# Kernel optimization log

Hardware: AMD Instinct MI355X
Metric: run time of the kernel (lower is better)

Reference implementation:

```python
import jax, jax.numpy as jnp
import numpy as np

TOTAL_BITS = 16
FRAC_BITS = 8
SCALE = float(2 ** FRAC_BITS)
MINV = -(2.0 ** (TOTAL_BITS - 1)) / SCALE          # -128.0
MAXV = (2.0 ** (TOTAL_BITS - 1) - 1.0) / SCALE     # 127.99609375
BN_EPS = 1e-5


def fp_quantize(x):
    """Fixed-point fake-quant: clamp to representable range, round to nearest
    multiple of 2^-frac_bits. Rounding uses straight-through estimator (matches
    the repo's RoundToFixedPoint autograd)."""
    x = jnp.clip(x, MINV, MAXV)
    r = jnp.round(x * SCALE) / SCALE
    return x + jax.lax.stop_gradient(r - x)


def setup_inputs() -> dict:
    key = jax.random.key(0)
    k1, k2, k3 = jax.random.split(key, 3)
    B, IN, OUT = 8192, 2048, 2048
    x = jax.random.normal(k1, (B, IN), dtype=jnp.float32)
    # realistic init scale so fixed-point range is exercised but not saturated
    weight = jax.random.normal(k2, (OUT, IN), dtype=jnp.float32) * 0.02
    bias = jax.random.normal(k3, (OUT,), dtype=jnp.float32) * 0.02
    gamma = jnp.ones((OUT,), dtype=jnp.float32)
    beta = jnp.zeros((OUT,), dtype=jnp.float32)
    return {"x": x, "weight": weight, "bias": bias, "gamma": gamma, "beta": beta}


def reference(x, weight, bias, gamma, beta):
    # fixed-point Linear: quantize params, quantized matmul, quantized add
    qw = fp_quantize(weight)            # [OUT, IN]
    qb = fp_quantize(bias)              # [OUT]
    y = fp_quantize(x @ qw.T)           # [B, OUT], arithmetics.matmul
    y = fp_quantize(y + qb)             # arithmetics.add
    # BatchNorm1d, training mode: biased batch statistics over the batch dim
    mean = jnp.mean(y, axis=0)
    var = jnp.mean((y - mean) ** 2, axis=0)
    y = (y - mean) * jax.lax.rsqrt(var + BN_EPS)
    y = gamma * y + beta
    # final quantize of BN output
    return fp_quantize(y)
```

## Files before the change

### kernel.cpp

```cpp
#include <hip/hip_runtime.h>
#include <hip/hip_bf16.h>

#define Mdim 8192
#define Ndim 2048
#define Kdim 2048
#define NT   32

constexpr float kMin = -128.0f;
constexpr float kMax = 127.99609375f;
constexpr float kScale = 256.0f;
constexpr float kInvScale = 1.0f / 256.0f;
constexpr float kEps = 1e-5f;

typedef __attribute__((ext_vector_type(8))) short short8;
typedef __attribute__((ext_vector_type(4))) float f32x4;

__device__ __forceinline__ float fpq(float x) {
    x = fminf(fmaxf(x, kMin), kMax);
    return rintf(x * kScale) * kInvScale;
}

__device__ __forceinline__ unsigned short f2bf(float f) {
    union { __hip_bfloat16 h; unsigned short u; } cv;
    cv.h = __float2bfloat16(f);
    return cv.u;
}

__device__ __forceinline__ void gload_lds16(const void* g, void* l) {
    __builtin_amdgcn_global_load_lds(
        (const __attribute__((address_space(1))) unsigned int*)g,
        (__attribute__((address_space(3))) unsigned int*)l,
        16, 0, 0);
}

__global__ void fpbn_prep(const float* __restrict__ w,
                          unsigned short* __restrict__ wb,
                          const float* __restrict__ x,
                          unsigned short* __restrict__ xb,
                          float* __restrict__ stats) {
    const int b = blockIdx.x;
    if (b == 0) {
        float4 z = {0.f, 0.f, 0.f, 0.f};
        for (int i = threadIdx.x; i < 1024; i += 256)
            ((float4*)stats)[i] = z;
    }
    if (b < 1024) {
        const int n4 = Ndim * Kdim / 4;
        for (int i = b * 256 + threadIdx.x; i < n4; i += 1024 * 256) {
            float4 v = ((const float4*)w)[i];
            ushort4 o;
            o.x = f2bf(fpq(v.x));
            o.y = f2bf(fpq(v.y));
            o.z = f2bf(fpq(v.z));
            o.w = f2bf(fpq(v.w));
            ((ushort4*)wb)[i] = o;
        }
    } else {
        const int n8 = Mdim * Kdim / 8;
        for (int i = (b - 1024) * 256 + threadIdx.x; i < n8; i += 2048 * 256) {
            float4 p = ((const float4*)x)[2 * i];
            float4 q = ((const float4*)x)[2 * i + 1];
            uint4 o;
            o.x = (unsigned)f2bf(p.x) | ((unsigned)f2bf(p.y) << 16);
            o.y = (unsigned)f2bf(p.z) | ((unsigned)f2bf(p.w) << 16);
            o.z = (unsigned)f2bf(q.x) | ((unsigned)f2bf(q.y) << 16);
            o.w = (unsigned)f2bf(q.z) | ((unsigned)f2bf(q.w) << 16);
            ((uint4*)xb)[i] = o;
        }
    }
}

template <bool OUT16>
__global__ __launch_bounds__(512, 2) void fpbn_gemm8(
    const unsigned short* __restrict__ xb, const unsigned short* __restrict__ wb,
    const float* __restrict__ bias, short* __restrict__ y16,
    float* __restrict__ yf, float* __restrict__ colsum,
    float* __restrict__ colsumsq) {

    __shared__ unsigned short lds[65536];

    const int t    = threadIdx.x;
    const int lane = t & 63;
    const int w    = t >> 6;
    const int wm   = w >> 2;
    const int wn   = w & 3;

    const int blk  = blockIdx.x;
    const int bm   = (blk & 7) * 4 + (blk >> 6);
    const int bn   = (blk >> 3) & 7;
    const int row0 = bm * 256;
    const int col0 = bn * 256;

    const int roff = t >> 3;
    const int colE = ((t & 7) ^ (roff & 7)) * 8;
    const unsigned short* srcA[2] = {
        xb + (size_t)(row0 +   0 + roff) * Kdim + colE,
        xb + (size_t)(row0 + 128 + roff) * Kdim + colE };
    const unsigned short* srcB[2] = {
        wb + (size_t)(col0 +   0 + roff) * Kdim + colE,
        wb + (size_t)(col0 + 128 + roff) * Kdim + colE };
    const int t8 = t * 8;

    const int x3    = lane & 7;
    const int xk    = x3 >> 2;
    const int xh    = x3 & 3;
    const int hi    = lane >> 4;
    const int rb2   = (lane & 15) * 64 + ((hi ^ xh) * 8);
    const int k0off = xk * 32;
    const int k1off = 32 - k0off;
    const int bnoff = (wn & 1) * 4096;

#define STAGE(BUF_, S_, OP_, HALF_) do {                                      \
        int ss_ = (S_) < NT ? (S_) : (S_) - 2;  \
        const unsigned short* sp_ = (OP_ ? srcB : srcA)[HALF_] + ss_ * 64;    \
        unsigned short* dp_ =                                                 \
            &lds[(((BUF_) * 4 + (OP_) * 2 + (HALF_)) << 13) + t8];            \
        gload_lds16(sp_, dp_);                                                \
        gload_lds16(sp_ + (size_t)64 * Kdim, dp_ + 4096);                     \
    } while (0)

#define READA(BUF_, M_, KOFF_) \
    (*(const short8*)&lds[(((BUF_) * 4 + wm) << 13) + rb2 + (M_) * 1024 + (KOFF_)])
#define READB(BUF_, N_, KOFF_) \
    (*(const short8*)&lds[(((BUF_) * 4 + 2 + (wn >> 1)) << 13) + bnoff + rb2 + (N_) * 1024 + (KOFF_)])
#define MFMA_(A_, B_, C_) \
    C_ = __builtin_amdgcn_mfma_f32_16x16x32_bf16(A_, B_, C_, 0, 0, 0)

#define PH_OPEN                                                    \
    __builtin_amdgcn_s_barrier();                                  \
    asm volatile("s_waitcnt lgkmcnt(0)" ::: "memory");             \
    __builtin_amdgcn_sched_barrier(0);                             \
    __builtin_amdgcn_s_setprio(1);

#define PH_CLOSE                                                   \
    __builtin_amdgcn_s_setprio(0);                                 \
    __builtin_amdgcn_s_barrier();

#define GATE_VM6 asm volatile("s_waitcnt vmcnt(6)" ::: "memory")

    f32x4 acc[8][4] = {};

    STAGE(0, 0, 1, 0); STAGE(0, 0, 1, 1); STAGE(0, 0, 0, 0); STAGE(0, 0, 0, 1);
    STAGE(1, 1, 1, 0); STAGE(1, 1, 1, 1); STAGE(1, 1, 0, 0);
    GATE_VM6;
    __builtin_amdgcn_s_barrier();

#define KTILE(BUF_, SA1_, SB0_, SB1_, SA0_) do {                              \
                                     \
        _Pragma("unroll") for (int n = 0; n < 2; ++n) {                       \
            Bf0[n][0] = READB(BUF_, n, k0off);                                \
            Bf0[n][1] = READB(BUF_, n, k1off); }                              \
        _Pragma("unroll") for (int m = 0; m < 4; ++m) {                       \
            Af[m][0] = READA(BUF_, m, k0off);                                 \
            Af[m][1] = READA(BUF_, m, k1off); }                               \
        SA1_;                                                                 \
        PH_OPEN                                                               \
        _Pragma("unroll") for (int m = 0; m < 4; ++m)                         \
        _Pragma("unroll") for (int n = 0; n < 2; ++n) {                       \
            MFMA_(Af[m][0], Bf0[n][0], acc[m][n]);                            \
            MFMA_(Af[m][1], Bf0[n][1], acc[m][n]); }                          \
        PH_CLOSE                                                              \
                                              \
        _Pragma("unroll") for (int n = 0; n < 2; ++n) {                       \
            Bf1[n][0] = READB(BUF_, n + 2, k0off);                            \
            Bf1[n][1] = READB(BUF_, n + 2, k1off); }                          \
        PH_OPEN                                                               \
        _Pragma("unroll") for (int m = 0; m < 4; ++m)                         \
        _Pragma("unroll") for (int n = 0; n < 2; ++n) {                       \
            MFMA_(Af[m][0], Bf1[n][0], acc[m][n + 2]);                        \
            MFMA_(Af[m][1], Bf1[n][1], acc[m][n + 2]); }                      \
        PH_CLOSE                                                              \
              \
        _Pragma("unroll") for (int m = 0; m < 4; ++m) {                       \
            Af2[m][0] = READA(BUF_, m + 4, k0off);                            \
            Af2[m][1] = READA(BUF_, m + 4, k1off); }                          \
        SB0_;                                                                 \
        SB1_;                                                                 \
        PH_OPEN                                                               \
        _Pragma("unroll") for (int m = 0; m < 4; ++m)                         \
        _Pragma("unroll") for (int n = 0; n < 2; ++n) {                       \
            MFMA_(Af2[m][0], Bf1[n][0], acc[m + 4][n + 2]);                   \
            MFMA_(Af2[m][1], Bf1[n][1], acc[m + 4][n + 2]); }                 \
        PH_CLOSE                                                              \
            \
        SA0_;                                                                 \
        GATE_VM6;                                                             \
        PH_OPEN                                                               \
        _Pragma("unroll") for (int m = 0; m < 4; ++m)                         \
        _Pragma("unroll") for (int n = 0; n < 2; ++n) {                       \
            MFMA_(Af2[m][0], Bf0[n][0], acc[m + 4][n]);                       \
            MFMA_(Af2[m][1], Bf0[n][1], acc[m + 4][n]); }                     \
        PH_CLOSE                                                              \
    } while (0)

#pragma unroll 1
    for (int it = 0; it < NT / 2; ++it) {
        const int s0 = 2 * it;
        short8 Af[4][2], Af2[4][2], Bf0[2][2], Bf1[2][2];
        KTILE(0, STAGE(1, s0 + 1, 0, 1),
                 STAGE(0, s0 + 2, 1, 0), STAGE(0, s0 + 2, 1, 1),
                 STAGE(0, s0 + 2, 0, 0));
        KTILE(1, STAGE(0, s0 + 2, 0, 1),
                 STAGE(1, s0 + 3, 1, 0), STAGE(1, s0 + 3, 1, 1),
                 STAGE(1, s0 + 3, 0, 0));
    }
    asm volatile("s_waitcnt vmcnt(0)" ::: "memory");

#pragma unroll
    for (int n = 0; n < 4; ++n) {
        const int col = col0 + wn * 64 + n * 16 + (lane & 15);
        const float qb = fpq(bias[col]);
        float s = 0.0f, s2 = 0.0f;
#pragma unroll
        for (int m = 0; m < 8; ++m) {
            const int rowb = row0 + wm * 128 + m * 16 + ((lane >> 4) * 4);
#pragma unroll
            for (int j = 0; j < 4; ++j) {
                float v = fpq(acc[m][n][j]);
                v = fpq(v + qb);
                if constexpr (OUT16) {
                    size_t idx = ((((size_t)blk * 8 + w) * 4 + n) * 32
                                  + m * 4 + j) * 64 + lane;
                    y16[idx] = (short)(v * 256.0f);
                } else {
                    yf[(size_t)(rowb + j) * Ndim + col] = v;
                }
                s += v;
                s2 += v * v;
            }
        }
        s  += __shfl_xor(s, 16, 64);  s  += __shfl_xor(s, 32, 64);
        s2 += __shfl_xor(s2, 16, 64); s2 += __shfl_xor(s2, 32, 64);
        if (lane < 16) {
            atomicAdd(&colsum[col], s);
            atomicAdd(&colsumsq[col], s2);
        }
    }
#undef STAGE
#undef READA
#undef READB
#undef MFMA_
#undef KTILE
#undef PH_OPEN
#undef PH_CLOSE
#undef GATE_VM6
}

__global__ void fpbn_finalize(const float* __restrict__ colsum,
                              const float* __restrict__ colsumsq,
                              const float* __restrict__ gamma,
                              const float* __restrict__ beta,
                              float* __restrict__ a, float* __restrict__ b) {
    int i = blockIdx.x * blockDim.x + threadIdx.x;
    if (i < Ndim) {
        float mean = colsum[i] * (1.0f / Mdim);
        float var  = colsumsq[i] * (1.0f / Mdim) - mean * mean;
        float inv  = 1.0f / sqrtf(var + kEps);
        float ai   = gamma[i] * inv;
        a[i] = ai;
        b[i] = beta[i] - mean * ai;
    }
}

__global__ void fpbn_apply16(const short* __restrict__ y16,
                             float* __restrict__ out,
                             const float* __restrict__ a,
                             const float* __restrict__ b, int ngroups) {
    int tid = blockIdx.x * blockDim.x + threadIdx.x;
    int stride = gridDim.x * blockDim.x;
    for (int g = tid; g < ngroups; g += stride) {
        const int r  = g >> 8;
        const int c  = (g & 255) * 8;
        const int bm = r >> 8, wm = (r >> 7) & 1, m = (r >> 4) & 7,
                  hi = (r >> 2) & 3, j = r & 3;
        const int bn = c >> 8, wn = (c >> 6) & 3, n = (c >> 4) & 3,
                  lane = hi * 16 + (c & 15);
        const int blk = (bm >> 2) | (bn << 3) | ((bm & 3) << 6);
        const int w   = wm * 4 + wn;
        const size_t idx = ((((size_t)blk * 8 + w) * 4 + n) * 32
                            + m * 4 + j) * 64 + lane;
        int4 raw = *(const int4*)(y16 + idx);
        const short* sp = (const short*)&raw;
        float4 a0 = *(const float4*)&a[c], a1 = *(const float4*)&a[c + 4];
        float4 b0 = *(const float4*)&b[c], b1 = *(const float4*)&b[c + 4];
        float4 o0, o1;
        o0.x = fpq(fmaf(a0.x, (float)sp[0] * kInvScale, b0.x));
        o0.y = fpq(fmaf(a0.y, (float)sp[1] * kInvScale, b0.y));
        o0.z = fpq(fmaf(a0.z, (float)sp[2] * kInvScale, b0.z));
        o0.w = fpq(fmaf(a0.w, (float)sp[3] * kInvScale, b0.w));
        o1.x = fpq(fmaf(a1.x, (float)sp[4] * kInvScale, b1.x));
        o1.y = fpq(fmaf(a1.y, (float)sp[5] * kInvScale, b1.y));
        o1.z = fpq(fmaf(a1.z, (float)sp[6] * kInvScale, b1.z));
        o1.w = fpq(fmaf(a1.w, (float)sp[7] * kInvScale, b1.w));
        float* op = out + (size_t)r * Ndim + c;
        ((float4*)op)[0] = o0;
        ((float4*)op)[1] = o1;
    }
}

__global__ void fpbn_apply(float* __restrict__ y,
                           const float* __restrict__ a,
                           const float* __restrict__ b, int n4) {
    int i = blockIdx.x * blockDim.x + threadIdx.x;
    int stride = gridDim.x * blockDim.x;
    for (; i < n4; i += stride) {
        float4 v = ((float4*)y)[i];
        int cb = (i * 4) & (Ndim - 1);
        float4 av = *(const float4*)&a[cb];
        float4 bv = *(const float4*)&b[cb];
        v.x = fpq(fmaf(av.x, v.x, bv.x));
        v.y = fpq(fmaf(av.y, v.y, bv.y));
        v.z = fpq(fmaf(av.z, v.z, bv.z));
        v.w = fpq(fmaf(av.w, v.w, bv.w));
        ((float4*)y)[i] = v;
    }
}

extern "C" void kernel_launch(void* const* d_in, const int* in_sizes, int n_in,
                              void* d_out, int out_size, void* d_ws, size_t ws_size,
                              hipStream_t stream) {
    const float* x      = (const float*)d_in[0];
    const float* weight = (const float*)d_in[1];
    const float* bias   = (const float*)d_in[2];
    const float* gamma  = (const float*)d_in[3];
    const float* beta   = (const float*)d_in[4];
    float* out = (float*)d_out;

    char* ws = (char*)d_ws;
    unsigned short* wb = (unsigned short*)ws;
    const size_t wbBytes = (size_t)Ndim * Kdim * 2;
    float* colsum   = (float*)(ws + wbBytes);
    float* colsumsq = colsum + Ndim;
    float* aArr     = colsum + 2 * Ndim;
    float* bArr     = colsum + 3 * Ndim;
    const size_t xbOff = wbBytes + 65536;
    unsigned short* xb = (unsigned short*)(ws + xbOff);
    const size_t xbBytes  = (size_t)Mdim * Kdim * 2;
    const size_t y16Off   = xbOff + xbBytes;
    short* y16 = (short*)(ws + y16Off);
    const size_t need16 = y16Off + (size_t)Mdim * Ndim * 2;

    fpbn_prep<<<3072, 256, 0, stream>>>(weight, wb, x, xb, colsum);

    if (ws_size >= need16) {
        fpbn_gemm8<true><<<(Mdim / 256) * (Ndim / 256), 512, 0, stream>>>(
            xb, wb, bias, y16, nullptr, colsum, colsumsq);
        fpbn_finalize<<<(Ndim + 255) / 256, 256, 0, stream>>>(
            colsum, colsumsq, gamma, beta, aArr, bArr);
        fpbn_apply16<<<2048, 256, 0, stream>>>(y16, out, aArr, bArr,
                                               Mdim * Ndim / 8);
    } else {
        fpbn_gemm8<false><<<(Mdim / 256) * (Ndim / 256), 512, 0, stream>>>(
            xb, wb, bias, nullptr, out, colsum, colsumsq);
        fpbn_finalize<<<(Ndim + 255) / 256, 256, 0, stream>>>(
            colsum, colsumsq, gamma, beta, aArr, bArr);
        fpbn_apply<<<2048, 256, 0, stream>>>(out, aArr, bArr, Mdim * Ndim / 4);
    }
}
```

Baseline: 215.5 us.

## Software-pipeline LDS fragment reads behind MFMA phases with ping-pong registers

```diff
diff --git a/kernel.cpp b/kernel.cpp
--- a/kernel.cpp
+++ b/kernel.cpp
@@ -140,67 +140,76 @@
 
     f32x4 acc[8][4] = {};
 
-    STAGE(0, 0, 1, 0); STAGE(0, 0, 1, 1); STAGE(0, 0, 0, 0); STAGE(0, 0, 0, 1);
+    STAGE(0, 0, 0, 0); STAGE(0, 0, 0, 1); STAGE(0, 0, 1, 0); STAGE(0, 0, 1, 1);
     STAGE(1, 1, 1, 0); STAGE(1, 1, 1, 1); STAGE(1, 1, 0, 0);
     GATE_VM6;
     __builtin_amdgcn_s_barrier();
 
-#define KTILE(BUF_, SA1_, SB0_, SB1_, SA0_) do {                              \
-                                     \
-        _Pragma("unroll") for (int n = 0; n < 2; ++n) {                       \
-            Bf0[n][0] = READB(BUF_, n, k0off);                                \
-            Bf0[n][1] = READB(BUF_, n, k1off); }                              \
-        _Pragma("unroll") for (int m = 0; m < 4; ++m) {                       \
-            Af[m][0] = READA(BUF_, m, k0off);                                 \
-            Af[m][1] = READA(BUF_, m, k1off); }                               \
-        SA1_;                                                                 \
+    short8 X[4][2], Y[4][2], B0r[2][2], B1r[2][2];
+#pragma unroll
+    for (int m = 0; m < 4; ++m) {
+        X[m][0] = READA(0, m, k0off);
+        X[m][1] = READA(0, m, k1off);
+    }
+#pragma unroll
+    for (int n = 0; n < 2; ++n) {
+        B0r[n][0] = READB(0, n, k0off);
+        B0r[n][1] = READB(0, n, k1off);
+    }
+
+#define KTILE(BUF_, A0_, A1_, SA1_, SB0_, SB1_, SA0_) do {                    \
+                   \
         PH_OPEN                                                               \
         _Pragma("unroll") for (int m = 0; m < 4; ++m)                         \
         _Pragma("unroll") for (int n = 0; n < 2; ++n) {                       \
-            MFMA_(Af[m][0], Bf0[n][0], acc[m][n]);                            \
-            MFMA_(Af[m][1], Bf0[n][1], acc[m][n]); }                          \
+            MFMA_(A0_[m][0], B0r[n][0], acc[m][n]);                           \
+            MFMA_(A0_[m][1], B0r[n][1], acc[m][n]); }                         \
+        _Pragma("unroll") for (int m = 0; m < 4; ++m) {                       \
+            A1_[m][0] = READA(BUF_, m + 4, k0off);                            \
+            A1_[m][1] = READA(BUF_, m + 4, k1off); }                          \
         PH_CLOSE                                                              \
-                                              \
-        _Pragma("unroll") for (int n = 0; n < 2; ++n) {                       \
-            Bf1[n][0] = READB(BUF_, n + 2, k0off);                            \
-            Bf1[n][1] = READB(BUF_, n + 2, k1off); }                          \
+        SA1_;                                                                 \
+                      \
         PH_OPEN                                                               \
         _Pragma("unroll") for (int m = 0; m < 4; ++m)                         \
         _Pragma("unroll") for (int n = 0; n < 2; ++n) {                       \
-            MFMA_(Af[m][0], Bf1[n][0], acc[m][n + 2]);                        \
-            MFMA_(Af[m][1], Bf1[n][1], acc[m][n + 2]); }                      \
+            MFMA_(A1_[m][0], B0r[n][0], acc[m + 4][n]);                       \
+            MFMA_(A1_[m][1], B0r[n][1], acc[m + 4][n]); }                     \
+        _Pragma("unroll") for (int n = 0; n < 2; ++n) {                       \
+            B1r[n][0] = READB(BUF_, n + 2, k0off);                            \
+            B1r[n][1] = READB(BUF_, n + 2, k1off); }                          \
         PH_CLOSE                                                              \
-              \
-        _Pragma("unroll") for (int m = 0; m < 4; ++m) {                       \
-            Af2[m][0] = READA(BUF_, m + 4, k0off);                            \
-            Af2[m][1] = READA(BUF_, m + 4, k1off); }                          \
-        SB0_;                                                                 \
-        SB1_;                                                                 \
+                      \
         PH_OPEN                                                               \
         _Pragma("unroll") for (int m = 0; m < 4; ++m)                         \
         _Pragma("unroll") for (int n = 0; n < 2; ++n) {                       \
-            MFMA_(Af2[m][0], Bf1[n][0], acc[m + 4][n + 2]);                   \
-            MFMA_(Af2[m][1], Bf1[n][1], acc[m + 4][n + 2]); }                 \
+            MFMA_(A1_[m][0], B1r[n][0], acc[m + 4][n + 2]);                   \
+            MFMA_(A1_[m][1], B1r[n][1], acc[m + 4][n + 2]); }                 \
         PH_CLOSE                                                              \
+        SB0_; SB1_; SA0_;                                                     \
+        GATE_VM6;                                                             \
             \
-        SA0_;                                                                 \
-        GATE_VM6;                                                             \
         PH_OPEN                                                               \
         _Pragma("unroll") for (int m = 0; m < 4; ++m)                         \
         _Pragma("unroll") for (int n = 0; n < 2; ++n) {                       \
-            MFMA_(Af2[m][0], Bf0[n][0], acc[m + 4][n]);                       \
-            MFMA_(Af2[m][1], Bf0[n][1], acc[m + 4][n]); }                     \
+            MFMA_(A0_[m][0], B1r[n][0], acc[m][n + 2]);                       \
+            MFMA_(A0_[m][1], B1r[n][1], acc[m][n + 2]); }                     \
+        _Pragma("unroll") for (int m = 0; m < 4; ++m) {                       \
+            A1_[m][0] = READA((BUF_) ^ 1, m, k0off);                          \
+            A1_[m][1] = READA((BUF_) ^ 1, m, k1off); }                        \
+        _Pragma("unroll") for (int n = 0; n < 2; ++n) {                       \
+            B0r[n][0] = READB((BUF_) ^ 1, n, k0off);                          \
+            B0r[n][1] = READB((BUF_) ^ 1, n, k1off); }                        \
         PH_CLOSE                                                              \
     } while (0)
 
 #pragma unroll 1
     for (int it = 0; it < NT / 2; ++it) {
         const int s0 = 2 * it;
-        short8 Af[4][2], Af2[4][2], Bf0[2][2], Bf1[2][2];
-        KTILE(0, STAGE(1, s0 + 1, 0, 1),
+        KTILE(0, X, Y, STAGE(1, s0 + 1, 0, 1),
                  STAGE(0, s0 + 2, 1, 0), STAGE(0, s0 + 2, 1, 1),
                  STAGE(0, s0 + 2, 0, 0));
-        KTILE(1, STAGE(0, s0 + 2, 0, 1),
+        KTILE(1, Y, X, STAGE(0, s0 + 2, 0, 1),
                  STAGE(1, s0 + 3, 1, 0), STAGE(1, s0 + 3, 1, 1),
                  STAGE(1, s0 + 3, 0, 0));
     }
```

New measurement: 214.0 us. About the same (-0.7%).
